# Performance work log

Measured on AMD Instinct MI355X. Metric: run time of the kernel, lower is better.

Reference implementation:

```python
import jax, jax.numpy as jnp
import numpy as np

B, CH1, CH2, HID, T, E = 64, 3, 4, 16, 16384, 512

def setup_inputs() -> dict:
    key = jax.random.key(0)
    ks = jax.random.split(key, 12)
    s_t = 1.0 / np.sqrt(T)   # fan_in = input_dim for q/k/v projections
    s_e = 1.0 / np.sqrt(E)   # fan_in = embed_dim for out_proj
    return {
        "x":  jax.random.normal(ks[0], (B, 7, T), jnp.float32),
        "W1": jax.random.normal(ks[1], (HID, CH1), jnp.float32) / np.sqrt(CH1),
        "W2": jax.random.normal(ks[2], (HID, CH2), jnp.float32) / np.sqrt(CH2),
        "Wq": jax.random.normal(ks[3], (E, T), jnp.float32) * s_t,
        "bq": jnp.zeros((E,), jnp.float32),
        "Wk": jax.random.normal(ks[4], (E, T), jnp.float32) * s_t,
        "bk": jnp.zeros((E,), jnp.float32),
        "Wv": jax.random.normal(ks[5], (E, T), jnp.float32) * s_t,
        "bv": jnp.zeros((E,), jnp.float32),
        "Wo": jax.random.normal(ks[6], (T, E), jnp.float32) * s_e,
        "bo": jnp.zeros((T,), jnp.float32),
        "W3": jax.random.normal(ks[7], (CH1, HID), jnp.float32) / np.sqrt(HID),
    }

def reference(x, W1, W2, Wq, bq, Wk, bk, Wv, bv, Wo, bo, W3):
    p = x[:, :CH1]            # [B,3,T]  narrow(1,0,ch_1)
    c = x[:, 3:3 + CH2]       # [B,4,T]  narrow(1,3,ch_2)
    q = jnp.einsum('oc,bct->bot', W1, p)   # fc_1: [B,16,T]
    cc = jnp.einsum('oc,bct->bot', W2, c)  # fc_2: [B,16,T]
    # CrossAttention: Linears act on last dim (T -> E)
    Q = jnp.einsum('bct,et->bce', q, Wq) + bq    # [B,16,E]
    K = jnp.einsum('bct,et->bce', cc, Wk) + bk   # [B,16,E]
    V = jnp.einsum('bct,et->bce', cc, Wv) + bv   # [B,16,E]
    scale = 1.0 / np.sqrt(HID)                   # nch = 16 query channels
    attn_w = jax.nn.softmax(jnp.einsum('bce,bcf->bef', Q, K) * scale, axis=-1)  # [B,E,E]
    attn = jnp.einsum('bef,bcf->bce', attn_w, V)  # [B,16,E]
    out = jnp.einsum('bce,te->bct', attn, Wo) + bo  # out_proj: [B,16,T]
    y = jnp.einsum('oc,bct->bot', W3, out)          # fc_3: [B,3,T]
    return p + y
```

## Files before the change

### kernel.cpp

```cpp
#include <hip/hip_runtime.h>

#define BB 64
#define TT 16384
#define EE 512

typedef _Float16 half8 __attribute__((ext_vector_type(8)));
typedef float floatx4 __attribute__((ext_vector_type(4)));

static __device__ __forceinline__ half8 cvt_half8(float4 a, float4 b) {
  half8 h;
  h[0] = (_Float16)a.x; h[1] = (_Float16)a.y; h[2] = (_Float16)a.z; h[3] = (_Float16)a.w;
  h[4] = (_Float16)b.x; h[5] = (_Float16)b.y; h[6] = (_Float16)b.z; h[7] = (_Float16)b.w;
  return h;
}

__global__ __launch_bounds__(256) void zero_ws(float4* __restrict__ p) {
  p[blockIdx.x * 256 + threadIdx.x] = (float4){0.f, 0.f, 0.f, 0.f};
}

__global__ __launch_bounds__(256) void proj_gemm(
    const float* __restrict__ x, const float* __restrict__ Wq,
    const float* __restrict__ Wk, const float* __restrict__ Wv,
    float* __restrict__ Xq, float* __restrict__ Xkv)
{
  __shared__ _Float16 As[64][40];
  __shared__ _Float16 Bs[128][40];
  const int t = threadIdx.x;
  const int wave = t >> 6, lane = t & 63;
  const int quad = lane >> 4, l16 = lane & 15;

  const int tile = blockIdx.x;
  int mtile, ntile, chan_base, cpb, ldout;
  const float *Wa, *Wb;
  float* outC;
  if (tile < 12) {
    mtile = tile >> 2; ntile = tile & 3;
    chan_base = 0; cpb = 3; ldout = 512;
    Wa = Wq; Wb = Wq; outC = Xq;
  } else {
    const int t2 = tile - 12;
    mtile = t2 >> 3; ntile = t2 & 7;
    chan_base = 3; cpb = 4; ldout = 1024;
    Wa = Wk; Wb = Wv; outC = Xkv;
  }
  const int k0 = blockIdx.y << 9;

  const int arow = t >> 2, akk = (t & 3) << 3;
  const int r = mtile * 64 + arow;
  const int bidx = r / cpb;
  const int j = r - bidx * cpb;
  const float* aptr = x + (size_t)(bidx * 7 + chan_base + j) * TT + k0 + akk;

  const int brow = t >> 1, bkk = (t & 1) << 4;
  const int ncol = ntile * 128 + brow;
  const float* wsrc = (ncol < EE) ? Wa : Wb;
  const float* bptr = wsrc + (size_t)(ncol & (EE - 1)) * TT + k0 + bkk;

  floatx4 acc[4][2];
  for (int rt = 0; rt < 4; ++rt)
    for (int ct = 0; ct < 2; ++ct)
      acc[rt][ct] = (floatx4){0.f, 0.f, 0.f, 0.f};

  float4 a0 = *(const float4*)aptr;
  float4 a1 = *(const float4*)(aptr + 4);
  float4 b0 = *(const float4*)bptr;
  float4 b1 = *(const float4*)(bptr + 4);
  float4 b2 = *(const float4*)(bptr + 8);
  float4 b3 = *(const float4*)(bptr + 12);

  for (int kt = 0; kt < 16; ++kt) {
    const half8 ha  = cvt_half8(a0, a1);
    const half8 hb0 = cvt_half8(b0, b1);
    const half8 hb1 = cvt_half8(b2, b3);
    __syncthreads();
    *(half8*)&As[arow][akk]     = ha;
    *(half8*)&Bs[brow][bkk]     = hb0;
    *(half8*)&Bs[brow][bkk + 8] = hb1;
    __syncthreads();
    if (kt < 15) {
      aptr += 32; bptr += 32;
      a0 = *(const float4*)aptr;
      a1 = *(const float4*)(aptr + 4);
      b0 = *(const float4*)bptr;
      b1 = *(const float4*)(bptr + 4);
      b2 = *(const float4*)(bptr + 8);
      b3 = *(const float4*)(bptr + 12);
    }
    half8 bf0 = *(const half8*)&Bs[wave * 32 + l16][quad * 8];
    half8 bf1 = *(const half8*)&Bs[wave * 32 + 16 + l16][quad * 8];
#pragma unroll
    for (int rt = 0; rt < 4; ++rt) {
      half8 af = *(const half8*)&As[rt * 16 + l16][quad * 8];
      acc[rt][0] = __builtin_amdgcn_mfma_f32_16x16x32_f16(af, bf0, acc[rt][0], 0, 0, 0);
      acc[rt][1] = __builtin_amdgcn_mfma_f32_16x16x32_f16(af, bf1, acc[rt][1], 0, 0, 0);
    }
  }
#pragma unroll
  for (int rt = 0; rt < 4; ++rt) {
#pragma unroll
    for (int ct = 0; ct < 2; ++ct) {
      const int gr = mtile * 64 + rt * 16 + quad * 4;
      const int gc = ntile * 128 + wave * 32 + ct * 16 + l16;
#pragma unroll
      for (int rg = 0; rg < 4; ++rg)
        atomicAdd(&outC[(size_t)(gr + rg) * ldout + gc], acc[rt][ct][rg]);
    }
  }
}

__global__ __launch_bounds__(256) void attn_mid(
    const float* __restrict__ Xq, const float* __restrict__ Xkv,
    const float* __restrict__ W1, const float* __restrict__ W2,
    const float* __restrict__ W3,
    const float* __restrict__ bq, const float* __restrict__ bk,
    const float* __restrict__ bv, _Float16* __restrict__ U)
{
  __shared__ float Ks[16][512];
  __shared__ float VW[3][512];
  __shared__ float Qs[16][64];
  __shared__ float Xs[4][512];
  __shared__ float W1s[48], W2s[64], W3s[48], W32s[12], w3sum[3];
  const int t = threadIdx.x;
  const int b = blockIdx.y;
  const int e0 = blockIdx.x * 64;

  if (t < 48) W1s[t] = W1[t];
  if (t >= 64 && t < 128) W2s[t - 64] = W2[t - 64];
  if (t >= 128 && t < 176) W3s[t - 128] = W3[t - 128];
  __syncthreads();
  if (t < 12) {
    const int o = t >> 2, jj = t & 3;
    float s = 0.f;
    for (int c = 0; c < 16; ++c) s += W3s[o * 16 + c] * W2s[c * 4 + jj];
    W32s[t] = s;
  }
  if (t >= 16 && t < 19) {
    const int o = t - 16;
    float s = 0.f;
    for (int c = 0; c < 16; ++c) s += W3s[o * 16 + c];
    w3sum[o] = s;
  }
  for (int i = t; i < 2048; i += 256) {
    const int jj = i >> 9, f = i & 511;
    Xs[jj][f] = Xkv[(size_t)(b * 4 + jj) * 1024 + f];
  }
  __syncthreads();
  for (int i = t; i < 8192; i += 256) {
    const int c = i >> 9, f = i & 511;
    float s = bk[f];
#pragma unroll
    for (int jj = 0; jj < 4; ++jj) s += W2s[c * 4 + jj] * Xs[jj][f];
    Ks[c][f] = s;
  }
  __syncthreads();
  for (int i = t; i < 2048; i += 256) {
    const int jj = i >> 9, f = i & 511;
    Xs[jj][f] = Xkv[(size_t)(b * 4 + jj) * 1024 + 512 + f];
  }
  __syncthreads();
  for (int i = t; i < 1536; i += 256) {
    const int o = i >> 9, f = i & 511;
    float s = w3sum[o] * bv[f];
#pragma unroll
    for (int jj = 0; jj < 4; ++jj) s += W32s[o * 4 + jj] * Xs[jj][f];
    VW[o][f] = s;
  }
  for (int i = t; i < 1024; i += 256) {
    const int c = i >> 6, el = i & 63;
    float s = bq[e0 + el];
#pragma unroll
    for (int jj = 0; jj < 3; ++jj)
      s += W1s[c * 3 + jj] * Xq[(size_t)(b * 3 + jj) * 512 + e0 + el];
    Qs[c][el] = s;
  }
  __syncthreads();

  const int wave = t >> 6, lane = t & 63;
  float vwr[3][8];
#pragma unroll
  for (int o = 0; o < 3; ++o) {
    float4 va = *(const float4*)&VW[o][lane * 8];
    float4 vb = *(const float4*)&VW[o][lane * 8 + 4];
    vwr[o][0] = va.x; vwr[o][1] = va.y; vwr[o][2] = va.z; vwr[o][3] = va.w;
    vwr[o][4] = vb.x; vwr[o][5] = vb.y; vwr[o][6] = vb.z; vwr[o][7] = vb.w;
  }

  for (int g = 0; g < 4; ++g) {
    const int el0 = wave * 16 + g * 4;
    float s[4][8];
#pragma unroll
    for (int e = 0; e < 4; ++e)
#pragma unroll
      for (int i = 0; i < 8; ++i) s[e][i] = 0.f;
#pragma unroll
    for (int c = 0; c < 16; ++c) {
      float4 k0 = *(const float4*)&Ks[c][lane * 8];
      float4 k1 = *(const float4*)&Ks[c][lane * 8 + 4];
      float4 qv = *(const float4*)&Qs[c][el0];
      float qa[4] = {qv.x, qv.y, qv.z, qv.w};
#pragma unroll
      for (int e = 0; e < 4; ++e) {
        const float q = qa[e];
        s[e][0] += q * k0.x; s[e][1] += q * k0.y; s[e][2] += q * k0.z; s[e][3] += q * k0.w;
        s[e][4] += q * k1.x; s[e][5] += q * k1.y; s[e][6] += q * k1.z; s[e][7] += q * k1.w;
      }
    }
#pragma unroll
    for (int e = 0; e < 4; ++e) {
      float mx = s[e][0];
#pragma unroll
      for (int i = 1; i < 8; ++i) mx = fmaxf(mx, s[e][i]);
#pragma unroll
      for (int off = 32; off; off >>= 1) mx = fmaxf(mx, __shfl_xor(mx, off));
      float p[8], sum = 0.f;
#pragma unroll
      for (int i = 0; i < 8; ++i) { p[i] = __expf(0.25f * (s[e][i] - mx)); sum += p[i]; }
      float u0 = 0.f, u1 = 0.f, u2 = 0.f;
#pragma unroll
      for (int i = 0; i < 8; ++i) {
        u0 += p[i] * vwr[0][i];
        u1 += p[i] * vwr[1][i];
        u2 += p[i] * vwr[2][i];
      }
#pragma unroll
      for (int off = 32; off; off >>= 1) {
        sum += __shfl_xor(sum, off);
        u0  += __shfl_xor(u0, off);
        u1  += __shfl_xor(u1, off);
        u2  += __shfl_xor(u2, off);
      }
      if (lane == 0) {
        const float inv = 1.0f / sum;
        const size_t base = (size_t)b * 3 * 512 + (e0 + el0 + e);
        U[base]        = (_Float16)(u0 * inv);
        U[base + 512]  = (_Float16)(u1 * inv);
        U[base + 1024] = (_Float16)(u2 * inv);
      }
    }
  }
}

__global__ __launch_bounds__(256) void out_gemm(
    const _Float16* __restrict__ U, const float* __restrict__ Wo,
    const float* __restrict__ x, const float* __restrict__ bo,
    const float* __restrict__ W3, float* __restrict__ outY)
{
  __shared__ _Float16 As[64][40];
  __shared__ _Float16 Bs[64][40];
  __shared__ float w3sh[3];
  const int t = threadIdx.x;
  const int wave = t >> 6, lane = t & 63;
  const int quad = lane >> 4, l16 = lane & 15;
  const int mtile = blockIdx.y, ntile = blockIdx.x;
  if (t < 3) {
    float s = 0.f;
    for (int c = 0; c < 16; ++c) s += W3[t * 16 + c];
    w3sh[t] = s;
  }
  const int arow = t >> 2, akk = (t & 3) << 3;
  const _Float16* aptr = U + (size_t)(mtile * 64 + arow) * EE + akk;
  const int brow = t >> 2, bkk = (t & 3) << 3;
  const float* bptr = Wo + (size_t)(ntile * 64 + brow) * EE + bkk;

  floatx4 acc[4];
  for (int rt = 0; rt < 4; ++rt) acc[rt] = (floatx4){0.f, 0.f, 0.f, 0.f};

  half8 av = *(const half8*)aptr;
  float4 b0 = *(const float4*)bptr;
  float4 b1 = *(const float4*)(bptr + 4);

  for (int kt = 0; kt < 16; ++kt) {
    const half8 hb = cvt_half8(b0, b1);
    const half8 ha = av;
    __syncthreads();
    *(half8*)&As[arow][akk] = ha;
    *(half8*)&Bs[brow][bkk] = hb;
    __syncthreads();
    if (kt < 15) {
      aptr += 32; bptr += 32;
      av = *(const half8*)aptr;
      b0 = *(const float4*)bptr;
      b1 = *(const float4*)(bptr + 4);
    }
    half8 bf = *(const half8*)&Bs[wave * 16 + l16][quad * 8];
#pragma unroll
    for (int rt = 0; rt < 4; ++rt) {
      half8 af = *(const half8*)&As[rt * 16 + l16][quad * 8];
      acc[rt] = __builtin_amdgcn_mfma_f32_16x16x32_f16(af, bf, acc[rt], 0, 0, 0);
    }
  }
#pragma unroll
  for (int rt = 0; rt < 4; ++rt) {
    const int gr = mtile * 64 + rt * 16 + quad * 4;
    const int tc = ntile * 64 + wave * 16 + l16;
    const float bot = bo[tc];
#pragma unroll
    for (int rg = 0; rg < 4; ++rg) {
      const int rr = gr + rg;
      const int bb = rr / 3, oo = rr - bb * 3;
      const float v = acc[rt][rg]
                    + x[(size_t)(bb * 7 + oo) * TT + tc]
                    + w3sh[oo] * bot;
      outY[(size_t)rr * TT + tc] = v;
    }
  }
}

extern "C" void kernel_launch(void* const* d_in, const int* in_sizes, int n_in,
                              void* d_out, int out_size, void* d_ws, size_t ws_size,
                              hipStream_t stream) {
  const float* x  = (const float*)d_in[0];
  const float* W1 = (const float*)d_in[1];
  const float* W2 = (const float*)d_in[2];
  const float* Wq = (const float*)d_in[3];
  const float* bq = (const float*)d_in[4];
  const float* Wk = (const float*)d_in[5];
  const float* bk = (const float*)d_in[6];
  const float* Wv = (const float*)d_in[7];
  const float* bv = (const float*)d_in[8];
  const float* Wo = (const float*)d_in[9];
  const float* bo = (const float*)d_in[10];
  const float* W3 = (const float*)d_in[11];
  float* out = (float*)d_out;

  char* ws = (char*)d_ws;
  float* Xq      = (float*)ws;
  float* Xkv     = (float*)(ws + 393216);
  _Float16* U    = (_Float16*)(ws + 1441792);

  zero_ws<<<dim3(352), 256, 0, stream>>>((float4*)ws);

  proj_gemm<<<dim3(44, 32), 256, 0, stream>>>(x, Wq, Wk, Wv, Xq, Xkv);
  attn_mid<<<dim3(8, BB), 256, 0, stream>>>(Xq, Xkv, W1, W2, W3, bq, bk, bv, U);
  out_gemm<<<dim3(256, 3), 256, 0, stream>>>(U, Wo, x, bo, W3, out);
}
```

Before: 276.1 us.

## Load MFMA fragments directly from global and split-K across waves in projection GEMM

```diff
diff --git a/kernel.cpp b/kernel.cpp
--- a/kernel.cpp
+++ b/kernel.cpp
@@ -23,88 +23,105 @@
     const float* __restrict__ Wk, const float* __restrict__ Wv,
     float* __restrict__ Xq, float* __restrict__ Xkv)
 {
-  __shared__ _Float16 As[64][40];
-  __shared__ _Float16 Bs[128][40];
+  __shared__ float red[4][2048];
   const int t = threadIdx.x;
   const int wave = t >> 6, lane = t & 63;
   const int quad = lane >> 4, l16 = lane & 15;
 
   const int tile = blockIdx.x;
   int mtile, ntile, chan_base, cpb, ldout;
-  const float *Wa, *Wb;
+  const float* Wsrc;
   float* outC;
-  if (tile < 12) {
-    mtile = tile >> 2; ntile = tile & 3;
+  if (tile < 48) {
+    mtile = tile >> 4; ntile = tile & 15;
     chan_base = 0; cpb = 3; ldout = 512;
-    Wa = Wq; Wb = Wq; outC = Xq;
+    Wsrc = Wq; outC = Xq;
   } else {
-    const int t2 = tile - 12;
-    mtile = t2 >> 3; ntile = t2 & 7;
+    const int t2 = tile - 48;
+    mtile = t2 >> 5; ntile = t2 & 31;
     chan_base = 3; cpb = 4; ldout = 1024;
-    Wa = Wk; Wb = Wv; outC = Xkv;
-  }
-  const int k0 = blockIdx.y << 9;
-
-  const int arow = t >> 2, akk = (t & 3) << 3;
-  const int r = mtile * 64 + arow;
-  const int bidx = r / cpb;
-  const int j = r - bidx * cpb;
-  const float* aptr = x + (size_t)(bidx * 7 + chan_base + j) * TT + k0 + akk;
-
-  const int brow = t >> 1, bkk = (t & 1) << 4;
-  const int ncol = ntile * 128 + brow;
-  const float* wsrc = (ncol < EE) ? Wa : Wb;
-  const float* bptr = wsrc + (size_t)(ncol & (EE - 1)) * TT + k0 + bkk;
+    Wsrc = (ntile < 16) ? Wk : Wv; outC = Xkv;
+  }
+  const int k0 = blockIdx.y * 2048 + wave * 512;
+
+  int aOff[4];
+#pragma unroll
+  for (int rt = 0; rt < 4; ++rt) {
+    const int r = mtile * 64 + rt * 16 + l16;
+    const int bidx = r / cpb;
+    const int j = r - bidx * cpb;
+    aOff[rt] = (bidx * 7 + chan_base + j) * TT + k0 + quad * 8;
+  }
+  int bOff[2];
+#pragma unroll
+  for (int ct = 0; ct < 2; ++ct) {
+    const int col = (ntile * 32 + ct * 16 + l16) & (EE - 1);
+    bOff[ct] = col * TT + k0 + quad * 8;
+  }
 
   floatx4 acc[4][2];
+#pragma unroll
   for (int rt = 0; rt < 4; ++rt)
+#pragma unroll
     for (int ct = 0; ct < 2; ++ct)
       acc[rt][ct] = (floatx4){0.f, 0.f, 0.f, 0.f};
 
-  float4 a0 = *(const float4*)aptr;
-  float4 a1 = *(const float4*)(aptr + 4);
-  float4 b0 = *(const float4*)bptr;
-  float4 b1 = *(const float4*)(bptr + 4);
-  float4 b2 = *(const float4*)(bptr + 8);
-  float4 b3 = *(const float4*)(bptr + 12);
+  float4 bufA[4][2], bufB[2][2];
+#pragma unroll
+  for (int rt = 0; rt < 4; ++rt) {
+    bufA[rt][0] = *(const float4*)(x + aOff[rt]);
+    bufA[rt][1] = *(const float4*)(x + aOff[rt] + 4);
+  }
+#pragma unroll
+  for (int ct = 0; ct < 2; ++ct) {
+    bufB[ct][0] = *(const float4*)(Wsrc + bOff[ct]);
+    bufB[ct][1] = *(const float4*)(Wsrc + bOff[ct] + 4);
+  }
 
   for (int kt = 0; kt < 16; ++kt) {
-    const half8 ha  = cvt_half8(a0, a1);
-    const half8 hb0 = cvt_half8(b0, b1);
-    const half8 hb1 = cvt_half8(b2, b3);
-    __syncthreads();
-    *(half8*)&As[arow][akk]     = ha;
-    *(half8*)&Bs[brow][bkk]     = hb0;
-    *(half8*)&Bs[brow][bkk + 8] = hb1;
-    __syncthreads();
+    half8 ha[4], hb[2];
+#pragma unroll
+    for (int rt = 0; rt < 4; ++rt) ha[rt] = cvt_half8(bufA[rt][0], bufA[rt][1]);
+#pragma unroll
+    for (int ct = 0; ct < 2; ++ct) hb[ct] = cvt_half8(bufB[ct][0], bufB[ct][1]);
     if (kt < 15) {
-      aptr += 32; bptr += 32;
-      a0 = *(const float4*)aptr;
-      a1 = *(const float4*)(aptr + 4);
-      b0 = *(const float4*)bptr;
-      b1 = *(const float4*)(bptr + 4);
-      b2 = *(const float4*)(bptr + 8);
-      b3 = *(const float4*)(bptr + 12);
-    }
-    half8 bf0 = *(const half8*)&Bs[wave * 32 + l16][quad * 8];
-    half8 bf1 = *(const half8*)&Bs[wave * 32 + 16 + l16][quad * 8];
+      const int ko = (kt + 1) * 32;
+#pragma unroll
+      for (int rt = 0; rt < 4; ++rt) {
+        bufA[rt][0] = *(const float4*)(x + aOff[rt] + ko);
+        bufA[rt][1] = *(const float4*)(x + aOff[rt] + ko + 4);
+      }
+#pragma unroll
+      for (int ct = 0; ct < 2; ++ct) {
+        bufB[ct][0] = *(const float4*)(Wsrc + bOff[ct] + ko);
+        bufB[ct][1] = *(const float4*)(Wsrc + bOff[ct] + ko + 4);
+      }
+    }
 #pragma unroll
     for (int rt = 0; rt < 4; ++rt) {
-      half8 af = *(const half8*)&As[rt * 16 + l16][quad * 8];
-      acc[rt][0] = __builtin_amdgcn_mfma_f32_16x16x32_f16(af, bf0, acc[rt][0], 0, 0, 0);
-      acc[rt][1] = __builtin_amdgcn_mfma_f32_16x16x32_f16(af, bf1, acc[rt][1], 0, 0, 0);
-    }
-  }
-#pragma unroll
-  for (int rt = 0; rt < 4; ++rt) {
-#pragma unroll
-    for (int ct = 0; ct < 2; ++ct) {
-      const int gr = mtile * 64 + rt * 16 + quad * 4;
-      const int gc = ntile * 128 + wave * 32 + ct * 16 + l16;
-#pragma unroll
-      for (int rg = 0; rg < 4; ++rg)
-        atomicAdd(&outC[(size_t)(gr + rg) * ldout + gc], acc[rt][ct][rg]);
-    }
+      acc[rt][0] = __builtin_amdgcn_mfma_f32_16x16x32_f16(ha[rt], hb[0], acc[rt][0], 0, 0, 0);
+      acc[rt][1] = __builtin_amdgcn_mfma_f32_16x16x32_f16(ha[rt], hb[1], acc[rt][1], 0, 0, 0);
+    }
+  }
+
+#pragma unroll
+  for (int rt = 0; rt < 4; ++rt)
+#pragma unroll
+    for (int ct = 0; ct < 2; ++ct)
+#pragma unroll
+      for (int rg = 0; rg < 4; ++rg) {
+        const int row = rt * 16 + quad * 4 + rg;
+        const int col = ct * 16 + l16;
+        red[wave][row * 32 + col] = acc[rt][ct][rg];
+      }
+  __syncthreads();
+  const int base = t * 8;
+#pragma unroll
+  for (int i = 0; i < 8; ++i) {
+    const int idx = base + i;
+    const float s = red[0][idx] + red[1][idx] + red[2][idx] + red[3][idx];
+    const int row = idx >> 5, col = idx & 31;
+    atomicAdd(&outC[(size_t)(mtile * 64 + row) * ldout + ntile * 32 + col], s);
   }
 }
 
@@ -245,62 +262,67 @@
     const float* __restrict__ x, const float* __restrict__ bo,
     const float* __restrict__ W3, float* __restrict__ outY)
 {
-  __shared__ _Float16 As[64][40];
-  __shared__ _Float16 Bs[64][40];
-  __shared__ float w3sh[3];
   const int t = threadIdx.x;
   const int wave = t >> 6, lane = t & 63;
   const int quad = lane >> 4, l16 = lane & 15;
   const int mtile = blockIdx.y, ntile = blockIdx.x;
-  if (t < 3) {
+
+  float w3s[3];
+#pragma unroll
+  for (int o = 0; o < 3; ++o) {
     float s = 0.f;
-    for (int c = 0; c < 16; ++c) s += W3[t * 16 + c];
-    w3sh[t] = s;
-  }
-  const int arow = t >> 2, akk = (t & 3) << 3;
-  const _Float16* aptr = U + (size_t)(mtile * 64 + arow) * EE + akk;
-  const int brow = t >> 2, bkk = (t & 3) << 3;
-  const float* bptr = Wo + (size_t)(ntile * 64 + brow) * EE + bkk;
+#pragma unroll
+    for (int c = 0; c < 16; ++c) s += W3[o * 16 + c];
+    w3s[o] = s;
+  }
+
+  const int tc = ntile * 64 + wave * 16 + l16;
+  int aOff[4];
+#pragma unroll
+  for (int rt = 0; rt < 4; ++rt)
+    aOff[rt] = (mtile * 64 + rt * 16 + l16) * EE + quad * 8;
+  const int bOff = tc * EE + quad * 8;
 
   floatx4 acc[4];
+#pragma unroll
   for (int rt = 0; rt < 4; ++rt) acc[rt] = (floatx4){0.f, 0.f, 0.f, 0.f};
 
-  half8 av = *(const half8*)aptr;
-  float4 b0 = *(const float4*)bptr;
-  float4 b1 = *(const float4*)(bptr + 4);
+  half8 bufA[4];
+  float4 bufB[2];
+#pragma unroll
+  for (int rt = 0; rt < 4; ++rt) bufA[rt] = *(const half8*)(U + aOff[rt]);
+  bufB[0] = *(const float4*)(Wo + bOff);
+  bufB[1] = *(const float4*)(Wo + bOff + 4);
 
   for (int kt = 0; kt < 16; ++kt) {
-    const half8 hb = cvt_half8(b0, b1);
-    const half8 ha = av;
-    __syncthreads();
-    *(half8*)&As[arow][akk] = ha;
-    *(half8*)&Bs[brow][bkk] = hb;
-    __syncthreads();
+    const half8 hb = cvt_half8(bufB[0], bufB[1]);
+    half8 ha[4];
+#pragma unroll
+    for (int rt = 0; rt < 4; ++rt) ha[rt] = bufA[rt];
     if (kt < 15) {
-      aptr += 32; bptr += 32;
-      av = *(const half8*)aptr;
-      b0 = *(const float4*)bptr;
-      b1 = *(const float4*)(bptr + 4);
-    }
-    half8 bf = *(const half8*)&Bs[wave * 16 + l16][quad * 8];
-#pragma unroll
-    for (int rt = 0; rt < 4; ++rt) {
-      half8 af = *(const half8*)&As[rt * 16 + l16][quad * 8];
-      acc[rt] = __builtin_amdgcn_mfma_f32_16x16x32_f16(af, bf, acc[rt], 0, 0, 0);
-    }
-  }
+      const int ko = (kt + 1) * 32;
+#pragma unroll
+      for (int rt = 0; rt < 4; ++rt)
+        bufA[rt] = *(const half8*)(U + aOff[rt] + ko);
+      bufB[0] = *(const float4*)(Wo + bOff + ko);
+      bufB[1] = *(const float4*)(Wo + bOff + ko + 4);
+    }
+#pragma unroll
+    for (int rt = 0; rt < 4; ++rt)
+      acc[rt] = __builtin_amdgcn_mfma_f32_16x16x32_f16(ha[rt], hb, acc[rt], 0, 0, 0);
+  }
+
+  const float bot = bo[tc];
 #pragma unroll
   for (int rt = 0; rt < 4; ++rt) {
     const int gr = mtile * 64 + rt * 16 + quad * 4;
-    const int tc = ntile * 64 + wave * 16 + l16;
-    const float bot = bo[tc];
 #pragma unroll
     for (int rg = 0; rg < 4; ++rg) {
       const int rr = gr + rg;
       const int bb = rr / 3, oo = rr - bb * 3;
       const float v = acc[rt][rg]
                     + x[(size_t)(bb * 7 + oo) * TT + tc]
-                    + w3sh[oo] * bot;
+                    + w3s[oo] * bot;
       outY[(size_t)rr * TT + tc] = v;
     }
   }
@@ -330,7 +352,7 @@
 
   zero_ws<<<dim3(352), 256, 0, stream>>>((float4*)ws);
 
-  proj_gemm<<<dim3(44, 32), 256, 0, stream>>>(x, Wq, Wk, Wv, Xq, Xkv);
+  proj_gemm<<<dim3(176, 8), 256, 0, stream>>>(x, Wq, Wk, Wv, Xq, Xkv);
   attn_mid<<<dim3(8, BB), 256, 0, stream>>>(Xq, Xkv, W1, W2, W3, bq, bk, bv, U);
   out_gemm<<<dim3(256, 3), 256, 0, stream>>>(U, Wo, x, bo, W3, out);
 }
```

Result: slower. 374.1 us (+35.5%).
